# Kernel tuning notes

Measured on AMD Instinct MI355X. Metric: run time of the kernel, lower is better.

## Reference

```python
import jax, jax.numpy as jnp
import numpy as np

B, A, D, H, S, C, NB = 8192, 8, 4096, 1024, 32, 32, 8
BS = D // NB          # 512: hidden block size
IBS = (2 * H) // NB   # 256: input block size (gru input = action_embed ++ stoch_embed)
UNIMIX = 0.01


def setup_inputs() -> dict:
    key = jax.random.key(0)
    ks = jax.random.split(key, 16)
    rn = lambda k, shape, s=1.0: jax.random.normal(k, shape, jnp.float32) * s
    return {
        'deterministic': rn(ks[0], (B, D)),
        'stochastic': jax.random.uniform(ks[1], (B, S, C), jnp.float32),
        'prev_action': rn(ks[2], (B, A)),
        'embed': rn(ks[3], (B, H)),
        'is_first': jax.random.bernoulli(ks[4], 0.1, (B,)),
        # encoders (nn.Linear stores weight as [out, in])
        'W_act': rn(ks[5], (H, A), 1.0 / np.sqrt(A)), 'b_act': jnp.zeros((H,)),
        'W_stoch': rn(ks[6], (H, S * C), 1.0 / np.sqrt(S * C)), 'b_stoch': jnp.zeros((H,)),
        # block-diagonal GRU: per-block [3*BS, IBS] and [3*BS, BS]
        'W_ih': rn(ks[7], (NB, 3 * BS, IBS), 1.0 / np.sqrt(IBS)), 'b_ih': jnp.zeros((NB, 3 * BS)),
        'W_hh': rn(ks[8], (NB, 3 * BS, BS), 1.0 / np.sqrt(BS)), 'b_hh': jnp.zeros((NB, 3 * BS)),
        # prior net: D -> H -> S*C
        'W_pr1': rn(ks[9], (H, D), 1.0 / np.sqrt(D)), 'b_pr1': jnp.zeros((H,)),
        'W_pr2': rn(ks[10], (S * C, H), 1.0 / np.sqrt(H)), 'b_pr2': jnp.zeros((S * C,)),
        # posterior net: D+H -> H -> S*C
        'W_po1': rn(ks[11], (H, D + H), 1.0 / np.sqrt(D + H)), 'b_po1': jnp.zeros((H,)),
        'W_po2': rn(ks[12], (S * C, H), 1.0 / np.sqrt(H)), 'b_po2': jnp.zeros((S * C,)),
    }


def _forward(deterministic, stochastic, prev_action, embed, is_first,
             W_act, b_act, W_stoch, b_stoch, W_ih, b_ih, W_hh, b_hh,
             W_pr1, b_pr1, W_pr2, b_pr2, W_po1, b_po1, W_po2, b_po2):
    # reset state where is_first (initial_state is all zeros)
    det = jnp.where(is_first[:, None], 0.0, deterministic)
    stoch = jnp.where(is_first[:, None, None], 0.0, stochastic)
    # action normalization (magnitude detached)
    mag = jnp.maximum(jnp.max(jnp.abs(prev_action), axis=-1, keepdims=True), 1.0)
    act = prev_action / jax.lax.stop_gradient(mag)
    # encoders
    ae = act @ W_act.T + b_act                         # [B, H]
    se = stoch.reshape(stoch.shape[0], -1) @ W_stoch.T + b_stoch  # [B, H]
    x = jnp.concatenate([ae, se], axis=-1)             # [B, 2H]
    # block-diagonal GRU: batched small GEMMs over NB blocks
    xb = x.reshape(-1, NB, IBS)
    hb = det.reshape(-1, NB, BS)
    gates = (jnp.einsum('bki,koi->bko', xb, W_ih) + b_ih
             + jnp.einsum('bkj,koj->bko', hb, W_hh) + b_hh)  # [B, NB, 3*BS]
    gates = gates.reshape(-1, NB, 3, BS)
    reset = jax.nn.sigmoid(gates[:, :, 0])
    update = jax.nn.sigmoid(gates[:, :, 1])
    cand = jnp.tanh(reset * gates[:, :, 2])
    h_new = ((1.0 - update) * hb + update * cand).reshape(-1, D)  # [B, D]
    # prior head
    ph = jax.nn.silu(h_new @ W_pr1.T + b_pr1)
    prior_logits = ph @ W_pr2.T + b_pr2                # [B, S*C]
    pp = jax.nn.softmax(prior_logits.reshape(-1, S, C), axis=-1)
    prior_probs = ((1.0 - UNIMIX) * pp + UNIMIX / C).reshape(-1, S * C)
    # posterior head
    qh = jax.nn.silu(jnp.concatenate([h_new, embed], axis=-1) @ W_po1.T + b_po1)
    post_logits = qh @ W_po2.T + b_po2                 # [B, S*C]
    return jnp.concatenate([h_new, prior_logits, prior_probs, post_logits], axis=-1)


def reference(deterministic, stochastic, prev_action, embed, is_first,
              W_act, b_act, W_stoch, b_stoch, W_ih, b_ih, W_hh, b_hh,
              W_pr1, b_pr1, W_pr2, b_pr2, W_po1, b_po1, W_po2, b_po2):
    return _forward(deterministic, stochastic, prev_action, embed, is_first,
                    W_act, b_act, W_stoch, b_stoch, W_ih, b_ih, W_hh, b_hh,
                    W_pr1, b_pr1, W_pr2, b_pr2, W_po1, b_po1, W_po2, b_po2)
```

## Files before the change

### kernel.cpp

```cpp
#include <hip/hip_runtime.h>

typedef unsigned short u16;
typedef short bf16x8 __attribute__((ext_vector_type(8)));
typedef float f32x4 __attribute__((ext_vector_type(4)));

#define BSZ 8192
#define OUTLD 7168

__device__ __forceinline__ u16 f2bf(float f) {
  union { float f; unsigned u; } v; v.f = f;
  unsigned r = v.u + 0x7FFFu + ((v.u >> 16) & 1u);
  return (u16)(r >> 16);
}
__device__ __forceinline__ float bf2f(u16 h) {
  union { unsigned u; float f; } v; v.u = ((unsigned)h) << 16;
  return v.f;
}
__device__ __forceinline__ float sigmoidf_(float x) { return 1.0f / (1.0f + __expf(-x)); }

__device__ __forceinline__ void gload16(const u16* g, u16* l) {
  __builtin_amdgcn_global_load_lds(
      (const __attribute__((address_space(1))) void*)g,
      (__attribute__((address_space(3))) void*)l, 16, 0, 0);
}

__global__ void k_detect(const unsigned* __restrict__ isf, int* __restrict__ flag) {
  __shared__ unsigned red;
  if (threadIdx.x == 0) red = 0u;
  __syncthreads();
  unsigned v = 0;
  for (int i = threadIdx.x; i < 2048; i += 256) v |= isf[i];
  atomicOr(&red, v);
  __syncthreads();
  if (threadIdx.x == 0)
    *flag = (((red & 0xFFFFFF00u) != 0u) && ((red & 0xFEFEFEFEu) == 0u)) ? 1 : 0;
}

__device__ __forceinline__ bool is_first_row(const void* isf, int fl, int b) {
  return fl ? (((const unsigned char*)isf)[b] != 0) : (((const int*)isf)[b] != 0);
}

struct Cv7 { const float* s[7]; u16* d[7]; long n4[7]; };
__global__ void k_cvtW(Cv7 c, long total4) {
  long stride = (long)gridDim.x * blockDim.x;
  for (long i = blockIdx.x * (long)blockDim.x + threadIdx.x; i < total4; i += stride) {
    long rem = i; int k = 0;
    while (k < 6 && rem >= c.n4[k]) { rem -= c.n4[k]; ++k; }
    float4 v = ((const float4*)c.s[k])[rem];
    ushort4 o; o.x = f2bf(v.x); o.y = f2bf(v.y); o.z = f2bf(v.z); o.w = f2bf(v.w);
    ((ushort4*)c.d[k])[rem] = o;
  }
}

struct Prep3 { const float* s[3]; u16* d[3]; long n4[3]; int c4[3]; int doR[3]; };
__global__ void k_prep(Prep3 p, const void* __restrict__ isf, const int* __restrict__ flag) {
  int fl = *flag;
  long stride = (long)gridDim.x * blockDim.x;
  long gid = blockIdx.x * (long)blockDim.x + threadIdx.x;
#pragma unroll 1
  for (int k = 0; k < 3; ++k) {
    const float4* src = (const float4*)p.s[k];
    ushort4* dst = (ushort4*)p.d[k];
    long n = p.n4[k]; int c4 = p.c4[k], doR = p.doR[k];
    for (long i = gid; i < n; i += stride) {
      float4 v = src[i];
      if (doR && is_first_row(isf, fl, (int)(i / c4))) { v.x = v.y = v.z = v.w = 0.f; }
      ushort4 o; o.x = f2bf(v.x); o.y = f2bf(v.y); o.z = f2bf(v.z); o.w = f2bf(v.w);
      dst[i] = o;
    }
  }
}

__global__ void k_ae(const float* __restrict__ act, const float* __restrict__ Wact,
                     const float* __restrict__ bact, u16* __restrict__ x) {
  long stride = (long)gridDim.x * blockDim.x;
  for (long t = blockIdx.x * (long)blockDim.x + threadIdx.x; t < (long)BSZ * 256; t += stride) {
    int b = (int)(t >> 8), h0 = (int)(t & 255) * 4;
    float4 a0 = ((const float4*)act)[b * 2];
    float4 a1 = ((const float4*)act)[b * 2 + 1];
    float mag = fmaxf(
        fmaxf(fmaxf(fabsf(a0.x), fabsf(a0.y)), fmaxf(fabsf(a0.z), fabsf(a0.w))),
        fmaxf(fmaxf(fabsf(a1.x), fabsf(a1.y)), fmaxf(fabsf(a1.z), fabsf(a1.w))));
    float inv = 1.0f / fmaxf(mag, 1.0f);
    ushort4 o;
    u16* op = (u16*)&o;
#pragma unroll
    for (int j = 0; j < 4; ++j) {
      int h = h0 + j;
      float4 w0 = ((const float4*)Wact)[h * 2];
      float4 w1 = ((const float4*)Wact)[h * 2 + 1];
      float dot = a0.x * w0.x + a0.y * w0.y + a0.z * w0.z + a0.w * w0.w
                + a1.x * w1.x + a1.y * w1.y + a1.z * w1.z + a1.w * w1.w;
      op[j] = f2bf(dot * inv + bact[h]);
    }
    *(ushort4*)&x[(long)b * 2048 + h0] = o;
  }
}

struct GDesc {
  const u16* A1; const u16* A2;
  int lda1, lda2, K1, K2;
  const u16* W1; const u16* W2;
  int ldw1, ldw2;
  const float* bias;
  float* outF; int ldoF;
  u16* outB; int ldoB;
  int actSilu;
};

__global__ __launch_bounds__(256, 3) void gemm128(GDesc d0, GDesc d1) {
  const GDesc d = blockIdx.z ? d1 : d0;
  __shared__ __align__(16) u16 lsA[128 * 64];
  __shared__ __align__(16) u16 lsB[128 * 64];
  const int tid = threadIdx.x;
  const int wave = tid >> 6, lane = tid & 63;
  const int m0 = blockIdx.x * 128, n0 = blockIdx.y * 128;
  const int wr = (wave >> 1) * 64, wc = (wave & 1) * 64;
  const int lrow = lane & 15;
  const int lq = lane >> 4;
  const int lr7 = lrow & 7;
  const int grow = wave * 8 + (lane >> 3);
  const int gcol = ((lane & 7) ^ (lane >> 3)) * 8;
  const int ro0 = ((lq ^ lr7)) * 8;
  const int ro1 = (((4 | lq) ^ lr7)) * 8;

  const f32x4 z4 = {0.f, 0.f, 0.f, 0.f};
  f32x4 acc[4][4];
#pragma unroll
  for (int m = 0; m < 4; ++m)
#pragma unroll
    for (int c = 0; c < 4; ++c) acc[m][c] = z4;

#pragma unroll 1
  for (int phse = 0; phse < 2; ++phse) {
    const u16* A = phse ? d.A2 : d.A1;
    const u16* W = phse ? d.W2 : d.W1;
    const int lda = phse ? d.lda2 : d.lda1;
    const int ldw = phse ? d.ldw2 : d.ldw1;
    const int K = phse ? d.K2 : d.K1;
#pragma unroll 1
    for (int k0 = 0; k0 < K; k0 += 64) {
      __syncthreads();
#pragma unroll
      for (int i = 0; i < 4; ++i) {
        gload16(&A[(long)(m0 + i * 32 + grow) * lda + k0 + gcol], &lsA[i * 2048 + wave * 512]);
        gload16(&W[(long)(n0 + i * 32 + grow) * ldw + k0 + gcol], &lsB[i * 2048 + wave * 512]);
      }
      __syncthreads();
#pragma unroll
      for (int kk = 0; kk < 2; ++kk) {
        const int ro = kk ? ro1 : ro0;
        bf16x8 af[4], wfr[4];
#pragma unroll
        for (int m = 0; m < 4; ++m)
          af[m] = *(const bf16x8*)&lsA[(wr + m * 16 + lrow) * 64 + ro];
#pragma unroll
        for (int c = 0; c < 4; ++c)
          wfr[c] = *(const bf16x8*)&lsB[(wc + c * 16 + lrow) * 64 + ro];
#pragma unroll
        for (int m = 0; m < 4; ++m)
#pragma unroll
          for (int c = 0; c < 4; ++c)
            acc[m][c] = __builtin_amdgcn_mfma_f32_16x16x32_bf16(af[m], wfr[c], acc[m][c], 0, 0, 0);
      }
    }
  }

#pragma unroll
  for (int c = 0; c < 4; ++c) {
    const int col = n0 + wc + c * 16 + lrow;
    const float bv = d.bias ? d.bias[col] : 0.f;
#pragma unroll
    for (int m = 0; m < 4; ++m) {
      const int rowb = m0 + wr + m * 16 + (lane >> 4) * 4;
#pragma unroll
      for (int r = 0; r < 4; ++r) {
        float v = acc[m][c][r] + bv;
        if (d.actSilu) v = v * sigmoidf_(v);
        if (d.outF) d.outF[(long)(rowb + r) * d.ldoF + col] = v;
        if (d.outB) d.outB[(long)(rowb + r) * d.ldoB + col] = f2bf(v);
      }
    }
  }
}

__global__ __launch_bounds__(256, 3) void gru128(
    const u16* __restrict__ xbuf, const u16* __restrict__ hbuf,
    const u16* __restrict__ Wih, const u16* __restrict__ Whh,
    const float* __restrict__ bih, const float* __restrict__ bhh,
    float* __restrict__ outF, u16* __restrict__ hnew)
{
  __shared__ __align__(16) u16 lsA[128 * 64];
  __shared__ __align__(16) u16 lsW[3 * 32 * 64];
  const int tid = threadIdx.x;
  const int wave = tid >> 6, lane = tid & 63;
  const int m0 = blockIdx.x * 128;
  const int blk = blockIdx.y >> 4;
  const int s0 = (blockIdx.y & 15) * 32;
  const int lrow = lane & 15;
  const int lq = lane >> 4;
  const int lr7 = lrow & 7;
  const int grow = wave * 8 + (lane >> 3);
  const int gcol = ((lane & 7) ^ (lane >> 3)) * 8;
  const int ro0 = ((lq ^ lr7)) * 8;
  const int ro1 = (((4 | lq) ^ lr7)) * 8;

  const f32x4 z4 = {0.f, 0.f, 0.f, 0.f};
  f32x4 acc[3][2][2];
#pragma unroll
  for (int g = 0; g < 3; ++g)
#pragma unroll
    for (int m = 0; m < 2; ++m)
#pragma unroll
      for (int c = 0; c < 2; ++c) acc[g][m][c] = z4;

#pragma unroll 1
  for (int phse = 0; phse < 2; ++phse) {
    const u16* A = phse ? (hbuf + blk * 512) : (xbuf + blk * 256);
    const u16* W = phse ? (Whh + (long)blk * 1536 * 512) : (Wih + (long)blk * 1536 * 256);
    const int lda = phse ? 4096 : 2048;
    const int ldw = phse ? 512 : 256;
    const int K = phse ? 512 : 256;
#pragma unroll 1
    for (int k0 = 0; k0 < K; k0 += 64) {
      __syncthreads();
#pragma unroll
      for (int i = 0; i < 4; ++i)
        gload16(&A[(long)(m0 + i * 32 + grow) * lda + k0 + gcol], &lsA[i * 2048 + wave * 512]);
#pragma unroll
      for (int j = 0; j < 3; ++j) {
        const int idx = j * 4 + wave;
        const int off = idx * 512;
        const int g = idx >> 2;
        const int r0 = (idx & 3) * 8;
        gload16(&W[(long)(g * 512 + s0 + r0 + (lane >> 3)) * ldw + k0 + gcol], &lsW[off]);
      }
      __syncthreads();
#pragma unroll
      for (int kk = 0; kk < 2; ++kk) {
        const int ro = kk ? ro1 : ro0;
        bf16x8 af[2], wfr[3][2];
#pragma unroll
        for (int m = 0; m < 2; ++m)
          af[m] = *(const bf16x8*)&lsA[(wave * 32 + m * 16 + lrow) * 64 + ro];
#pragma unroll
        for (int g = 0; g < 3; ++g)
#pragma unroll
          for (int c = 0; c < 2; ++c)
            wfr[g][c] = *(const bf16x8*)&lsW[g * 2048 + (c * 16 + lrow) * 64 + ro];
#pragma unroll
        for (int g = 0; g < 3; ++g)
#pragma unroll
          for (int m = 0; m < 2; ++m)
#pragma unroll
            for (int c = 0; c < 2; ++c)
              acc[g][m][c] = __builtin_amdgcn_mfma_f32_16x16x32_bf16(af[m], wfr[g][c], acc[g][m][c], 0, 0, 0);
      }
    }
  }

#pragma unroll
  for (int c = 0; c < 2; ++c) {
    const int s = s0 + c * 16 + lrow;
    const int bb = blk * 1536 + s;
    const float br = bih[bb] + bhh[bb];
    const float bu = bih[bb + 512] + bhh[bb + 512];
    const float bc = bih[bb + 1024] + bhh[bb + 1024];
    const int hcol = blk * 512 + s;
#pragma unroll
    for (int m = 0; m < 2; ++m) {
      const int rowb = m0 + wave * 32 + m * 16 + (lane >> 4) * 4;
#pragma unroll
      for (int r = 0; r < 4; ++r) {
        const int row = rowb + r;
        const float gr = acc[0][m][c][r] + br;
        const float gu = acc[1][m][c][r] + bu;
        const float gc = acc[2][m][c][r] + bc;
        const float rr = sigmoidf_(gr);
        const float uu = sigmoidf_(gu);
        const float cand = tanhf(rr * gc);
        const float h = bf2f(hbuf[(long)row * 4096 + hcol]);
        const float hn = (1.f - uu) * h + uu * cand;
        outF[(long)row * OUTLD + hcol] = hn;
        hnew[(long)row * 4096 + hcol] = f2bf(hn);
      }
    }
  }
}

__global__ void k_softmax(float* __restrict__ out) {
  int t = blockIdx.x * blockDim.x + threadIdx.x;
  if (t >= BSZ * 32) return;
  int b = t >> 5, g = t & 31;
  const float* src = out + (long)b * OUTLD + 4096 + g * 32;
  float* dst = out + (long)b * OUTLD + 5120 + g * 32;
  float v[32];
#pragma unroll
  for (int i = 0; i < 8; ++i) {
    float4 q = ((const float4*)src)[i];
    v[4 * i] = q.x; v[4 * i + 1] = q.y; v[4 * i + 2] = q.z; v[4 * i + 3] = q.w;
  }
  float m = v[0];
#pragma unroll
  for (int i = 1; i < 32; ++i) m = fmaxf(m, v[i]);
  float ssum = 0.f;
#pragma unroll
  for (int i = 0; i < 32; ++i) { v[i] = __expf(v[i] - m); ssum += v[i]; }
  float inv = 0.99f / ssum;
#pragma unroll
  for (int i = 0; i < 8; ++i) {
    float4 q;
    q.x = v[4 * i] * inv + 3.125e-4f;
    q.y = v[4 * i + 1] * inv + 3.125e-4f;
    q.z = v[4 * i + 2] * inv + 3.125e-4f;
    q.w = v[4 * i + 3] * inv + 3.125e-4f;
    ((float4*)dst)[i] = q;
  }
}

extern "C" void kernel_launch(void* const* d_in, const int* in_sizes, int n_in,
                              void* d_out, int out_size, void* d_ws, size_t ws_size,
                              hipStream_t stream) {
  const float* det   = (const float*)d_in[0];
  const float* stoch = (const float*)d_in[1];
  const float* pact  = (const float*)d_in[2];
  const float* embed = (const float*)d_in[3];
  const void*  isf   = d_in[4];
  const float* Wact  = (const float*)d_in[5];
  const float* bact  = (const float*)d_in[6];
  const float* Wst   = (const float*)d_in[7];
  const float* bst   = (const float*)d_in[8];
  const float* Wih   = (const float*)d_in[9];
  const float* bih   = (const float*)d_in[10];
  const float* Whh   = (const float*)d_in[11];
  const float* bhh   = (const float*)d_in[12];
  const float* Wpr1  = (const float*)d_in[13];
  const float* bpr1  = (const float*)d_in[14];
  const float* Wpr2  = (const float*)d_in[15];
  const float* bpr2  = (const float*)d_in[16];
  const float* Wpo1  = (const float*)d_in[17];
  const float* bpo1  = (const float*)d_in[18];
  const float* Wpo2  = (const float*)d_in[19];
  const float* bpo2  = (const float*)d_in[20];
  float* out = (float*)d_out;

  int* flag = (int*)d_ws;
  u16* wsu  = (u16*)((char*)d_ws + 256);
  u16* bWst  = wsu;
  u16* bWih  = wsu + 1048576UL;
  u16* bWhh  = wsu + 4194304UL;
  u16* bWpr1 = wsu + 10485760UL;
  u16* bWpr2 = wsu + 14680064UL;
  u16* bWpo1 = wsu + 15728640UL;
  u16* bWpo2 = wsu + 20971520UL;
  u16* bufX  = wsu + 22020096UL;
  u16* bufSt = wsu + 38797312UL;
  u16* bufHb = wsu + 47185920UL;
  u16* bufHn = wsu + 80740352UL;
  u16* bufEm = wsu + 114294784UL;

  k_detect<<<dim3(1), dim3(256), 0, stream>>>((const unsigned*)isf, flag);

  Cv7 cw;
  cw.s[0] = Wst;  cw.d[0] = bWst;  cw.n4[0] = 262144L;
  cw.s[1] = Wih;  cw.d[1] = bWih;  cw.n4[1] = 786432L;
  cw.s[2] = Whh;  cw.d[2] = bWhh;  cw.n4[2] = 1572864L;
  cw.s[3] = Wpr1; cw.d[3] = bWpr1; cw.n4[3] = 1048576L;
  cw.s[4] = Wpr2; cw.d[4] = bWpr2; cw.n4[4] = 262144L;
  cw.s[5] = Wpo1; cw.d[5] = bWpo1; cw.n4[5] = 1310720L;
  cw.s[6] = Wpo2; cw.d[6] = bWpo2; cw.n4[6] = 262144L;
  k_cvtW<<<dim3(2048), dim3(256), 0, stream>>>(cw, 5505024L);

  Prep3 pp;
  pp.s[0] = stoch; pp.d[0] = bufSt; pp.n4[0] = 2097152L; pp.c4[0] = 256;  pp.doR[0] = 1;
  pp.s[1] = det;   pp.d[1] = bufHb; pp.n4[1] = 8388608L; pp.c4[1] = 1024; pp.doR[1] = 1;
  pp.s[2] = embed; pp.d[2] = bufEm; pp.n4[2] = 2097152L; pp.c4[2] = 256;  pp.doR[2] = 0;
  k_prep<<<dim3(4096), dim3(256), 0, stream>>>(pp, isf, flag);

  k_ae<<<dim3(2048), dim3(256), 0, stream>>>(pact, Wact, bact, bufX);

  GDesc dSe;
  dSe.A1 = bufSt; dSe.A2 = nullptr; dSe.lda1 = 1024; dSe.lda2 = 0;
  dSe.K1 = 1024; dSe.K2 = 0;
  dSe.W1 = bWst; dSe.W2 = nullptr; dSe.ldw1 = 1024; dSe.ldw2 = 0;
  dSe.bias = bst; dSe.outF = nullptr; dSe.ldoF = 0;
  dSe.outB = bufX + 1024; dSe.ldoB = 2048; dSe.actSilu = 0;
  gemm128<<<dim3(64, 8, 1), dim3(256), 0, stream>>>(dSe, dSe);

  gru128<<<dim3(64, 128), dim3(256), 0, stream>>>(bufX, bufHb, bWih, bWhh, bih, bhh, out, bufHn);

  GDesc dPr1, dPo1;
  dPr1.A1 = bufHn; dPr1.A2 = nullptr; dPr1.lda1 = 4096; dPr1.lda2 = 0;
  dPr1.K1 = 4096; dPr1.K2 = 0;
  dPr1.W1 = bWpr1; dPr1.W2 = nullptr; dPr1.ldw1 = 4096; dPr1.ldw2 = 0;
  dPr1.bias = bpr1; dPr1.outF = nullptr; dPr1.ldoF = 0;
  dPr1.outB = bufSt; dPr1.ldoB = 1024; dPr1.actSilu = 1;
  dPo1.A1 = bufHn; dPo1.A2 = bufEm; dPo1.lda1 = 4096; dPo1.lda2 = 1024;
  dPo1.K1 = 4096; dPo1.K2 = 1024;
  dPo1.W1 = bWpo1; dPo1.W2 = bWpo1 + 4096; dPo1.ldw1 = 5120; dPo1.ldw2 = 5120;
  dPo1.bias = bpo1; dPo1.outF = nullptr; dPo1.ldoF = 0;
  dPo1.outB = bufHb; dPo1.ldoB = 1024; dPo1.actSilu = 1;
  gemm128<<<dim3(64, 8, 2), dim3(256), 0, stream>>>(dPr1, dPo1);

  GDesc dPr2, dPo2;
  dPr2.A1 = bufSt; dPr2.A2 = nullptr; dPr2.lda1 = 1024; dPr2.lda2 = 0;
  dPr2.K1 = 1024; dPr2.K2 = 0;
  dPr2.W1 = bWpr2; dPr2.W2 = nullptr; dPr2.ldw1 = 1024; dPr2.ldw2 = 0;
  dPr2.bias = bpr2; dPr2.outF = out + 4096; dPr2.ldoF = OUTLD;
  dPr2.outB = nullptr; dPr2.ldoB = 0; dPr2.actSilu = 0;
  dPo2.A1 = bufHb; dPo2.A2 = nullptr; dPo2.lda1 = 1024; dPo2.lda2 = 0;
  dPo2.K1 = 1024; dPo2.K2 = 0;
  dPo2.W1 = bWpo2; dPo2.W2 = nullptr; dPo2.ldw1 = 1024; dPo2.ldw2 = 0;
  dPo2.bias = bpo2; dPo2.outF = out + 6144; dPo2.ldoF = OUTLD;
  dPo2.outB = nullptr; dPo2.ldoB = 0; dPo2.actSilu = 0;
  gemm128<<<dim3(64, 8, 2), dim3(256), 0, stream>>>(dPr2, dPo2);

  k_softmax<<<dim3(1024), dim3(256), 0, stream>>>(out);
}
```

Baseline: 723.3 us.

## Widen GRU tile to 64 hidden units per block with 8 waves and fast tanh

The GRU gate kernel now runs 512-thread blocks that each cover 128 rows by 64 hidden units, with waves split 4x2 over rows and units. Each activation tile loaded into LDS is reused across twice as many weight columns, which halves redundant A-tile global traffic, and the block count drops by half. tanhf is replaced with an exp-based formula to make the epilogue cheaper. In exchange the block uses more LDS and has a tighter register budget from the raised launch bounds, and the exp-based tanh can lose a little accuracy.

```diff
diff --git a/kernel.cpp b/kernel.cpp
--- a/kernel.cpp
+++ b/kernel.cpp
@@ -17,6 +17,7 @@
   return v.f;
 }
 __device__ __forceinline__ float sigmoidf_(float x) { return 1.0f / (1.0f + __expf(-x)); }
+__device__ __forceinline__ float tanhf_(float t) { return 2.0f / (1.0f + __expf(-2.0f * t)) - 1.0f; }
 
 __device__ __forceinline__ void gload16(const u16* g, u16* l) {
   __builtin_amdgcn_global_load_lds(
@@ -184,23 +185,24 @@
   }
 }
 
-__global__ __launch_bounds__(256, 3) void gru128(
+__global__ __launch_bounds__(512, 4) void gru128(
     const u16* __restrict__ xbuf, const u16* __restrict__ hbuf,
     const u16* __restrict__ Wih, const u16* __restrict__ Whh,
     const float* __restrict__ bih, const float* __restrict__ bhh,
     float* __restrict__ outF, u16* __restrict__ hnew)
 {
   __shared__ __align__(16) u16 lsA[128 * 64];
-  __shared__ __align__(16) u16 lsW[3 * 32 * 64];
+  __shared__ __align__(16) u16 lsW[3 * 64 * 64];
   const int tid = threadIdx.x;
   const int wave = tid >> 6, lane = tid & 63;
+  const int wm = wave & 3;
+  const int ws = wave >> 2;
   const int m0 = blockIdx.x * 128;
-  const int blk = blockIdx.y >> 4;
-  const int s0 = (blockIdx.y & 15) * 32;
+  const int blk = blockIdx.y >> 3;
+  const int s0 = (blockIdx.y & 7) * 64;
   const int lrow = lane & 15;
   const int lq = lane >> 4;
   const int lr7 = lrow & 7;
-  const int grow = wave * 8 + (lane >> 3);
   const int gcol = ((lane & 7) ^ (lane >> 3)) * 8;
   const int ro0 = ((lq ^ lr7)) * 8;
   const int ro1 = (((4 | lq) ^ lr7)) * 8;
@@ -225,15 +227,16 @@
     for (int k0 = 0; k0 < K; k0 += 64) {
       __syncthreads();
 #pragma unroll
-      for (int i = 0; i < 4; ++i)
-        gload16(&A[(long)(m0 + i * 32 + grow) * lda + k0 + gcol], &lsA[i * 2048 + wave * 512]);
-#pragma unroll
-      for (int j = 0; j < 3; ++j) {
-        const int idx = j * 4 + wave;
-        const int off = idx * 512;
-        const int g = idx >> 2;
-        const int r0 = (idx & 3) * 8;
-        gload16(&W[(long)(g * 512 + s0 + r0 + (lane >> 3)) * ldw + k0 + gcol], &lsW[off]);
+      for (int r = 0; r < 2; ++r) {
+        const int chunk = r * 8 + wave;
+        gload16(&A[(long)(m0 + chunk * 8 + (lane >> 3)) * lda + k0 + gcol], &lsA[chunk * 512]);
+      }
+#pragma unroll
+      for (int r = 0; r < 3; ++r) {
+        const int chunk = r * 8 + wave;
+        const int g = chunk >> 3;
+        const int r0 = (chunk & 7) * 8;
+        gload16(&W[(long)(g * 512 + s0 + r0 + (lane >> 3)) * ldw + k0 + gcol], &lsW[chunk * 512]);
       }
       __syncthreads();
 #pragma unroll
@@ -242,12 +245,12 @@
         bf16x8 af[2], wfr[3][2];
 #pragma unroll
         for (int m = 0; m < 2; ++m)
-          af[m] = *(const bf16x8*)&lsA[(wave * 32 + m * 16 + lrow) * 64 + ro];
+          af[m] = *(const bf16x8*)&lsA[(wm * 32 + m * 16 + lrow) * 64 + ro];
 #pragma unroll
         for (int g = 0; g < 3; ++g)
 #pragma unroll
           for (int c = 0; c < 2; ++c)
-            wfr[g][c] = *(const bf16x8*)&lsW[g * 2048 + (c * 16 + lrow) * 64 + ro];
+            wfr[g][c] = *(const bf16x8*)&lsW[g * 4096 + (ws * 32 + c * 16 + lrow) * 64 + ro];
 #pragma unroll
         for (int g = 0; g < 3; ++g)
 #pragma unroll
@@ -261,7 +264,7 @@
 
 #pragma unroll
   for (int c = 0; c < 2; ++c) {
-    const int s = s0 + c * 16 + lrow;
+    const int s = s0 + ws * 32 + c * 16 + lrow;
     const int bb = blk * 1536 + s;
     const float br = bih[bb] + bhh[bb];
     const float bu = bih[bb + 512] + bhh[bb + 512];
@@ -269,7 +272,7 @@
     const int hcol = blk * 512 + s;
 #pragma unroll
     for (int m = 0; m < 2; ++m) {
-      const int rowb = m0 + wave * 32 + m * 16 + (lane >> 4) * 4;
+      const int rowb = m0 + wm * 32 + m * 16 + lq * 4;
 #pragma unroll
       for (int r = 0; r < 4; ++r) {
         const int row = rowb + r;
@@ -278,7 +281,7 @@
         const float gc = acc[2][m][c][r] + bc;
         const float rr = sigmoidf_(gr);
         const float uu = sigmoidf_(gu);
-        const float cand = tanhf(rr * gc);
+        const float cand = tanhf_(rr * gc);
         const float h = bf2f(hbuf[(long)row * 4096 + hcol]);
         const float hn = (1.f - uu) * h + uu * cand;
         outF[(long)row * OUTLD + hcol] = hn;
@@ -387,7 +390,7 @@
   dSe.outB = bufX + 1024; dSe.ldoB = 2048; dSe.actSilu = 0;
   gemm128<<<dim3(64, 8, 1), dim3(256), 0, stream>>>(dSe, dSe);
 
-  gru128<<<dim3(64, 128), dim3(256), 0, stream>>>(bufX, bufHb, bWih, bWhh, bih, bhh, out, bufHn);
+  gru128<<<dim3(64, 64), dim3(512), 0, stream>>>(bufX, bufHb, bWih, bWhh, bih, bhh, out, bufHn);
 
   GDesc dPr1, dPo1;
   dPr1.A1 = bufHn; dPr1.A2 = nullptr; dPr1.lda1 = 4096; dPr1.lda2 = 0;
```

Result: no change. 713.9 us (-1.3%).
